# Performance work log

Measured on AMD Instinct MI355X. Metric: run time of the kernel, lower is better.

## Reference

```python
import jax, jax.numpy as jnp
import numpy as np

H, D, E, FOCAL, HID = 8, 32, 16, 4, 256  # heads, att_size, edge types, focal heads, hidden
SCALE = D ** -0.5
B, N = 16, 512


def setup_inputs() -> dict:
    key = jax.random.key(0)
    ks = jax.random.split(key, 16)
    f = lambda i, shape, s=1.0: jax.random.normal(ks[i], shape, jnp.float32) * s
    return {
        "q": f(0, (B, N, HID)),
        "k": f(1, (B, N, HID)),
        "v": f(2, (B, N, HID)),
        "query_edge_emb": f(3, (E, H * D), 0.1),
        "key_edge_emb": f(4, (E, H * D), 0.1),
        "edge_attr": jax.random.randint(ks[5], (B, N, N), 0, E),
        "mask": jax.random.randint(ks[6], (B, N), 0, 2).astype(bool),
        "focal_mask": jax.random.randint(ks[7], (B, N, N), 0, 2).astype(bool),
        "Wq": f(8, (H * D, HID), 0.05), "bq": jnp.zeros((H * D,), jnp.float32),
        "Wk": f(9, (H * D, HID), 0.05), "bk": jnp.zeros((H * D,), jnp.float32),
        "Wv": f(10, (H * D, HID), 0.05), "bv": jnp.zeros((H * D,), jnp.float32),
        "Wo": f(11, (HID, H * D), 0.05), "bo": jnp.zeros((HID,), jnp.float32),
    }


def reference(q, k, v, query_edge_emb, key_edge_emb, edge_attr, mask, focal_mask,
              Wq, bq, Wk, bk, Wv, bv, Wo, bo):
    b, n, _ = q.shape
    # projections -> [B, H, N, D]
    qh = (q @ Wq.T + bq).reshape(b, n, H, D).transpose(0, 2, 1, 3)
    kh = (k @ Wk.T + bk).reshape(b, n, H, D).transpose(0, 2, 1, 3)
    vh = (v @ Wv.T + bv).reshape(b, n, H, D).transpose(0, 2, 1, 3)

    # edge-type embeddings -> [H, E, D]
    qe_emb = query_edge_emb.reshape(E, H, D).transpose(1, 0, 2)
    ke_emb = key_edge_emb.reshape(E, H, D).transpose(1, 0, 2)

    # per-node score against each edge type: [B, H, N, E]
    qe = jnp.einsum('bhnd,hed->bhne', qh, qe_emb)
    ke = jnp.einsum('bhnd,hed->bhne', kh, ke_emb)

    # gather per edge type id: [B, H, N, N]
    idx = jnp.broadcast_to(edge_attr[:, None, :, :], (b, H, n, n))
    edge_bias = jnp.take_along_axis(qe, idx, axis=3) + jnp.take_along_axis(ke, idx, axis=3)

    attn = (jnp.einsum('bhid,bhjd->bhij', qh, kh) + edge_bias) * SCALE

    gh = H - FOCAL
    m_g = jnp.broadcast_to(mask[:, None, None, :], (b, gh, n, n))
    m_f = jnp.broadcast_to(focal_mask[:, None, :, :], (b, FOCAL, n, n))
    m = jnp.concatenate([m_g, m_f], axis=1)
    attn = jnp.where(m, attn, -jnp.inf)
    attn = jax.nn.softmax(attn, axis=3)

    out = jnp.einsum('bhij,bhjd->bhid', attn, vh)
    out = out.transpose(0, 2, 1, 3).reshape(b, n, H * D)
    return out @ Wo.T + bo
```

## Files before the change

kernel.cpp:

```cpp
#include <hip/hip_runtime.h>
#include <math.h>

namespace {

constexpr int B = 16, N = 512, H = 8, D = 32, E = 16, HID = 256;
constexpr float SCALE = 0.17677669529663687f;
constexpr size_t HSZ = (size_t)B * H * N * D;
constexpr size_t WSZ = (size_t)HID * HID;
constexpr int CONV_BLOCKS = 6400;

typedef __attribute__((ext_vector_type(8))) short short8;
typedef __attribute__((ext_vector_type(4))) float float4v;

__device__ inline short f2bf(float x) {
  union { float f; unsigned u; } v; v.f = x;
  unsigned r = v.u + 0x7fffu + ((v.u >> 16) & 1u);
  return (short)(r >> 16);
}

__global__ __launch_bounds__(256) void prep_kernel(
    const float* __restrict__ q, const float* __restrict__ k, const float* __restrict__ v,
    const float* __restrict__ Wq, const float* __restrict__ Wk,
    const float* __restrict__ Wv, const float* __restrict__ Wo,
    unsigned short* __restrict__ qx, unsigned short* __restrict__ kx,
    unsigned short* __restrict__ vx, unsigned short* __restrict__ wq,
    unsigned short* __restrict__ wk, unsigned short* __restrict__ wv,
    unsigned short* __restrict__ wo,
    const int* __restrict__ ea, const void* __restrict__ maskp,
    const void* __restrict__ fmaskp, unsigned char* __restrict__ packed)
{
  __shared__ unsigned char tl[16 * 520];
  __shared__ unsigned sdet[4];
  const int bid = blockIdx.x, t = threadIdx.x;

  if (bid < CONV_BLOCKS) {
    constexpr size_t H4 = HSZ / 4;
    constexpr size_t W4 = WSZ / 4;
    const size_t idx = (size_t)bid * 256 + t;
    const float* src; unsigned short* dst; size_t off;
    if (idx < H4)            { src = q; dst = qx; off = idx; }
    else if (idx < 2 * H4)   { src = k; dst = kx; off = idx - H4; }
    else if (idx < 3 * H4)   { src = v; dst = vx; off = idx - 2 * H4; }
    else {
      const size_t r = idx - 3 * H4;
      const int wsel = (int)(r / W4); off = r % W4;
      src = (wsel == 0) ? Wq : (wsel == 1) ? Wk : (wsel == 2) ? Wv : Wo;
      dst = (wsel == 0) ? wq : (wsel == 1) ? wk : (wsel == 2) ? wv : wo;
    }
    const float4 f = ((const float4*)src)[off];
    ushort4 o;
    o.x = (unsigned short)f2bf(f.x); o.y = (unsigned short)f2bf(f.y);
    o.z = (unsigned short)f2bf(f.z); o.w = (unsigned short)f2bf(f.w);
    ((ushort4*)dst)[off] = o;
    return;
  }

  const int pb = bid - CONV_BLOCKS;
  const int it = pb & 31, b = pb >> 5;
  const int i0 = it * 16;
  const int w = t >> 6, lane = t & 63;
  const unsigned* fm_u = (const unsigned*)fmaskp;
  unsigned o = 0;
#pragma unroll
  for (int i = 0; i < 4; ++i) o |= fm_u[t + i * 256];
  o |= __shfl_xor(o, 1);  o |= __shfl_xor(o, 2);  o |= __shfl_xor(o, 4);
  o |= __shfl_xor(o, 8);  o |= __shfl_xor(o, 16); o |= __shfl_xor(o, 32);
  if (lane == 0) sdet[w] = o;
  __syncthreads();
  const int bf = ((sdet[0] | sdet[1] | sdet[2] | sdet[3]) > 1u) ? 1 : 0;

  const int* fm32 = (const int*)fmaskp;
  const unsigned char* fm8 = (const unsigned char*)fmaskp;
  const int* mk32 = (const int*)maskp;
  const unsigned char* mk8 = (const unsigned char*)maskp;

  for (int idx4 = t; idx4 < 2048; idx4 += 256) {
    const int m = idx4 >> 7, j4 = (idx4 & 127) * 4;
    const size_t rowoff = ((size_t)(b * N) + i0 + m) * N;
    const int4 e4 = *(const int4*)(ea + rowoff + j4);
    int fv0, fv1, fv2, fv3, mv0, mv1, mv2, mv3;
    if (bf) {
      const unsigned fw = *(const unsigned*)(fm8 + rowoff + j4);
      fv0 = fw & 0xff; fv1 = (fw >> 8) & 0xff; fv2 = (fw >> 16) & 0xff; fv3 = fw >> 24;
      const unsigned mw = *(const unsigned*)(mk8 + b * N + j4);
      mv0 = mw & 0xff; mv1 = (mw >> 8) & 0xff; mv2 = (mw >> 16) & 0xff; mv3 = mw >> 24;
    } else {
      const int4 fw = *(const int4*)(fm32 + rowoff + j4);
      fv0 = fw.x; fv1 = fw.y; fv2 = fw.z; fv3 = fw.w;
      const int4 mw = *(const int4*)(mk32 + b * N + j4);
      mv0 = mw.x; mv1 = mw.y; mv2 = mw.z; mv3 = mw.w;
    }
    const unsigned b0 = (e4.x & 15) | (fv0 ? 16u : 0u) | (mv0 ? 32u : 0u);
    const unsigned b1 = (e4.y & 15) | (fv1 ? 16u : 0u) | (mv1 ? 32u : 0u);
    const unsigned b2 = (e4.z & 15) | (fv2 ? 16u : 0u) | (mv2 ? 32u : 0u);
    const unsigned b3 = (e4.w & 15) | (fv3 ? 16u : 0u) | (mv3 ? 32u : 0u);
    *(unsigned*)&tl[m * 520 + j4] = b0 | (b1 << 8) | (b2 << 16) | (b3 << 24);
  }
  __syncthreads();
#pragma unroll
  for (int rep = 0; rep < 2; ++rep) {
    const int j = t * 2 + rep;
    unsigned wd[4];
#pragma unroll
    for (int g = 0; g < 4; ++g) {
      const unsigned c0 = tl[(g * 4 + 0) * 520 + j];
      const unsigned c1 = tl[(g * 4 + 1) * 520 + j];
      const unsigned c2 = tl[(g * 4 + 2) * 520 + j];
      const unsigned c3 = tl[(g * 4 + 3) * 520 + j];
      wd[g] = c0 | (c1 << 8) | (c2 << 16) | (c3 << 24);
    }
    *(uint4*)(packed + ((size_t)(b * 32 + it) * 512 + j) * 16) =
        make_uint4(wd[0], wd[1], wd[2], wd[3]);
  }
}

__global__ __launch_bounds__(256) void gemm_qkv(
    const unsigned short* __restrict__ Xq, const unsigned short* __restrict__ Xk,
    const unsigned short* __restrict__ Xv,
    const unsigned short* __restrict__ Wq, const unsigned short* __restrict__ Wk,
    const unsigned short* __restrict__ Wv,
    const float* __restrict__ bq, const float* __restrict__ bk,
    const float* __restrict__ bv,
    unsigned short* __restrict__ qh, unsigned short* __restrict__ kh,
    unsigned short* __restrict__ vt)
{
  __shared__ __align__(16) unsigned short As[64][72];
  __shared__ __align__(16) unsigned short Bs[64][72];
  const int z = blockIdx.z;
  const unsigned short* X = (z == 0) ? Xq : (z == 1) ? Xk : Xv;
  const unsigned short* W = (z == 0) ? Wq : (z == 1) ? Wk : Wv;
  const float* bias = (z == 0) ? bq : (z == 1) ? bk : bv;

  const int m0 = blockIdx.x * 64, n0 = blockIdx.y * 64;
  const int t = threadIdx.x, lane = t & 63, w = t >> 6;
  const int quad = lane >> 4, col = lane & 15;
  const int wm = (w & 1) * 32, wn = (w >> 1) * 32;
  const int srow = t >> 2, skk = (t & 3) * 16;
  float4v acc[2][2] = {{{0,0,0,0},{0,0,0,0}},{{0,0,0,0},{0,0,0,0}}};

  for (int kit = 0; kit < 4; ++kit) {
    const int k0 = kit * 64;
    {
      const unsigned short* xp = X + (size_t)(m0 + srow) * HID + k0 + skk;
      const unsigned short* wp = W + (size_t)(n0 + srow) * HID + k0 + skk;
      *(short8*)&As[srow][skk] = *(const short8*)xp;
      *(short8*)&As[srow][skk + 8] = *(const short8*)(xp + 8);
      *(short8*)&Bs[srow][skk] = *(const short8*)wp;
      *(short8*)&Bs[srow][skk + 8] = *(const short8*)(wp + 8);
    }
    __syncthreads();
#pragma unroll
    for (int ks = 0; ks < 2; ++ks) {
      const int kk = ks * 32 + quad * 8;
      short8 a0 = *(const short8*)&As[wm + col][kk];
      short8 a1 = *(const short8*)&As[wm + 16 + col][kk];
      short8 b0 = *(const short8*)&Bs[wn + col][kk];
      short8 b1 = *(const short8*)&Bs[wn + 16 + col][kk];
      acc[0][0] = __builtin_amdgcn_mfma_f32_16x16x32_bf16(a0, b0, acc[0][0], 0, 0, 0);
      acc[0][1] = __builtin_amdgcn_mfma_f32_16x16x32_bf16(a0, b1, acc[0][1], 0, 0, 0);
      acc[1][0] = __builtin_amdgcn_mfma_f32_16x16x32_bf16(a1, b0, acc[1][0], 0, 0, 0);
      acc[1][1] = __builtin_amdgcn_mfma_f32_16x16x32_bf16(a1, b1, acc[1][1], 0, 0, 0);
    }
    __syncthreads();
  }
  if (z == 2) {
#pragma unroll
    for (int mt = 0; mt < 2; ++mt)
#pragma unroll
      for (int nt = 0; nt < 2; ++nt)
#pragma unroll
        for (int r = 0; r < 4; ++r) {
          const int m_l = wm + mt * 16 + quad * 4 + r;
          const int n_l = wn + nt * 16 + col;
          As[n_l][m_l] = (unsigned short)f2bf(acc[mt][nt][r] + bias[n0 + n_l]);
        }
    __syncthreads();
#pragma unroll
    for (int rep = 0; rep < 16; ++rep) {
      const int flat = rep * 256 + t;
      const int n_l = flat >> 6, m_l = flat & 63;
      const int n = n0 + n_l, m = m0 + m_l;
      const int b_ = m >> 9, ii = m & 511, h_ = n >> 5, d_ = n & 31;
      vt[((size_t)(b_ * H + h_) * D + d_) * N + ii] = As[n_l][m_l];
    }
    return;
  }
#pragma unroll
  for (int mt = 0; mt < 2; ++mt)
#pragma unroll
    for (int nt = 0; nt < 2; ++nt)
#pragma unroll
      for (int r = 0; r < 4; ++r) {
        const int m = m0 + wm + mt * 16 + quad * 4 + r;
        const int n = n0 + wn + nt * 16 + col;
        const float val = acc[mt][nt][r] + bias[n];
        const int b_ = m >> 9, ii = m & 511, h_ = n >> 5, d_ = n & 31;
        unsigned short* Yh = (z == 0) ? qh : kh;
        Yh[((size_t)(b_ * H + h_) * N + ii) * D + d_] = (unsigned short)f2bf(val);
      }
}

__global__ __launch_bounds__(256) void gemm_out(
    const unsigned short* __restrict__ X, const unsigned short* __restrict__ W,
    const float* __restrict__ bias, float* __restrict__ Yf)
{
  __shared__ __align__(16) unsigned short As[64][72];
  __shared__ __align__(16) unsigned short Bs[64][72];
  const int m0 = blockIdx.x * 64, n0 = blockIdx.y * 64;
  const int t = threadIdx.x, lane = t & 63, w = t >> 6;
  const int quad = lane >> 4, col = lane & 15;
  const int wm = (w & 1) * 32, wn = (w >> 1) * 32;
  const int srow = t >> 2, skk = (t & 3) * 16;
  float4v acc[2][2] = {{{0,0,0,0},{0,0,0,0}},{{0,0,0,0},{0,0,0,0}}};

  for (int kit = 0; kit < 4; ++kit) {
    const int k0 = kit * 64;
    {
      const unsigned short* xp = X + (size_t)(m0 + srow) * HID + k0 + skk;
      const unsigned short* wp = W + (size_t)(n0 + srow) * HID + k0 + skk;
      *(short8*)&As[srow][skk] = *(const short8*)xp;
      *(short8*)&As[srow][skk + 8] = *(const short8*)(xp + 8);
      *(short8*)&Bs[srow][skk] = *(const short8*)wp;
      *(short8*)&Bs[srow][skk + 8] = *(const short8*)(wp + 8);
    }
    __syncthreads();
#pragma unroll
    for (int ks = 0; ks < 2; ++ks) {
      const int kk = ks * 32 + quad * 8;
      short8 a0 = *(const short8*)&As[wm + col][kk];
      short8 a1 = *(const short8*)&As[wm + 16 + col][kk];
      short8 b0 = *(const short8*)&Bs[wn + col][kk];
      short8 b1 = *(const short8*)&Bs[wn + 16 + col][kk];
      acc[0][0] = __builtin_amdgcn_mfma_f32_16x16x32_bf16(a0, b0, acc[0][0], 0, 0, 0);
      acc[0][1] = __builtin_amdgcn_mfma_f32_16x16x32_bf16(a0, b1, acc[0][1], 0, 0, 0);
      acc[1][0] = __builtin_amdgcn_mfma_f32_16x16x32_bf16(a1, b0, acc[1][0], 0, 0, 0);
      acc[1][1] = __builtin_amdgcn_mfma_f32_16x16x32_bf16(a1, b1, acc[1][1], 0, 0, 0);
    }
    __syncthreads();
  }
#pragma unroll
  for (int mt = 0; mt < 2; ++mt)
#pragma unroll
    for (int nt = 0; nt < 2; ++nt)
#pragma unroll
      for (int r = 0; r < 4; ++r) {
        const int m = m0 + wm + mt * 16 + quad * 4 + r;
        const int n = n0 + wn + nt * 16 + col;
        Yf[(size_t)m * HID + n] = acc[mt][nt][r] + bias[n];
      }
}

__global__ __launch_bounds__(256) void attn_mfma(
    const unsigned short* __restrict__ qh, const unsigned short* __restrict__ kh,
    const unsigned short* __restrict__ vt,
    const float* __restrict__ qemb, const float* __restrict__ kemb,
    const unsigned char* __restrict__ packed, unsigned short* __restrict__ ctx)
{
  __shared__ __align__(16) unsigned char SMEM[4][4352];
  __shared__ float qesS[2][16][17];
  __shared__ float2 wlm[4][2][16];
  __shared__ float scl[4][32];
  __shared__ float linv[32];

  const int it = blockIdx.x, p = blockIdx.y, b = blockIdx.z;
  const int i0 = it * 16;
  const int t = threadIdx.x, w = t >> 6, lane = t & 63;
  const int quad = lane >> 4, col = lane & 15;

  unsigned short* Pw = (unsigned short*)&SMEM[w][0];

  unsigned pk[8];
  {
    const unsigned char* pt = packed + ((size_t)(b * 32 + it) * 512) * 16;
#pragma unroll
    for (int c = 0; c < 8; ++c)
      pk[c] = *(const unsigned*)(pt + (size_t)(w * 128 + c * 16 + col) * 16 + quad * 4);
  }

  if (w < 2) {
    const int h2w = w;
    const int hp = p + h2w * 4;
    const int bhw = b * H + hp;
    const short8 qa = *(const short8*)(qh + ((size_t)bhw * N + i0 + col) * D + quad * 8);
    const short8 ka = *(const short8*)(kh + ((size_t)bhw * N + i0 + col) * D + quad * 8);
    const float* eqp = qemb + col * 256 + hp * 32 + quad * 8;
    const float* ekp = kemb + col * 256 + hp * 32 + quad * 8;
    const float4 e1 = *(const float4*)eqp, e2 = *(const float4*)(eqp + 4);
    const float4 k1 = *(const float4*)ekp, k2 = *(const float4*)(ekp + 4);
    short8 eb, kb;
    eb[0]=f2bf(e1.x); eb[1]=f2bf(e1.y); eb[2]=f2bf(e1.z); eb[3]=f2bf(e1.w);
    eb[4]=f2bf(e2.x); eb[5]=f2bf(e2.y); eb[6]=f2bf(e2.z); eb[7]=f2bf(e2.w);
    kb[0]=f2bf(k1.x); kb[1]=f2bf(k1.y); kb[2]=f2bf(k1.z); kb[3]=f2bf(k1.w);
    kb[4]=f2bf(k2.x); kb[5]=f2bf(k2.y); kb[6]=f2bf(k2.z); kb[7]=f2bf(k2.w);
    float4v qe = {0, 0, 0, 0};
    qe = __builtin_amdgcn_mfma_f32_16x16x32_bf16(qa, eb, qe, 0, 0, 0);
    qe = __builtin_amdgcn_mfma_f32_16x16x32_bf16(ka, kb, qe, 0, 0, 0);
#pragma unroll
    for (int r = 0; r < 4; ++r)
      qesS[h2w][quad * 4 + r][col] = qe[r] * SCALE;
  }
  __syncthreads();

  float4v oa[2][2] = {{{0,0,0,0},{0,0,0,0}},{{0,0,0,0},{0,0,0,0}}};
#pragma unroll
  for (int h2 = 0; h2 < 2; ++h2) {
    const int bh = b * H + p + h2 * 4;
    const short8 qf = *(const short8*)(qh + ((size_t)bh * N + i0 + col) * D + quad * 8);

    float s[8][4];
#pragma unroll
    for (int c = 0; c < 8; ++c) {
      const int j0 = w * 128 + c * 16;
      const short8 kf = *(const short8*)(kh + ((size_t)bh * N + j0 + col) * D + quad * 8);
      float4v sc = {0, 0, 0, 0};
      sc = __builtin_amdgcn_mfma_f32_16x16x32_bf16(qf, kf, sc, 0, 0, 0);
#pragma unroll
      for (int r = 0; r < 4; ++r) {
        const int m = quad * 4 + r;
        const unsigned by = pk[c] >> (8 * r);
        const int e = by & 15;
        const int valid = h2 ? (by >> 4) & 1 : (by >> 5) & 1;
        const float sv = fmaf(sc[r], SCALE, qesS[h2][m][e]);
        s[c][r] = valid ? sv : -INFINITY;
      }
    }

    float mW[4];
#pragma unroll
    for (int r = 0; r < 4; ++r) {
      float m2 = s[0][r];
#pragma unroll
      for (int c = 1; c < 8; ++c) m2 = fmaxf(m2, s[c][r]);
      m2 = fmaxf(m2, __shfl_xor(m2, 1));
      m2 = fmaxf(m2, __shfl_xor(m2, 2));
      m2 = fmaxf(m2, __shfl_xor(m2, 4));
      m2 = fmaxf(m2, __shfl_xor(m2, 8));
      mW[r] = fmaxf(m2, -3.0e38f);
    }
#pragma unroll
    for (int r = 0; r < 4; ++r) {
      const int m = quad * 4 + r;
      float sm = 0.f;
#pragma unroll
      for (int c = 0; c < 8; ++c) {
        const float ex = __expf(s[c][r] - mW[r]);
        sm += ex;
        Pw[m * 136 + c * 16 + col] = (unsigned short)f2bf(ex);
      }
      sm += __shfl_xor(sm, 1);
      sm += __shfl_xor(sm, 2);
      sm += __shfl_xor(sm, 4);
      sm += __shfl_xor(sm, 8);
      if (col == 0) wlm[w][h2][m] = make_float2(mW[r], sm);
    }

#pragma unroll
    for (int c2 = 0; c2 < 4; ++c2) {
      const int kl = c2 * 32 + quad * 8;
      const short8 pf = *(const short8*)&Pw[col * 136 + kl];
      const int kg = w * 128 + kl;
      const short8 v0 = *(const short8*)(vt + ((size_t)bh * D + col) * N + kg);
      const short8 v1 = *(const short8*)(vt + ((size_t)bh * D + 16 + col) * N + kg);
      oa[h2][0] = __builtin_amdgcn_mfma_f32_16x16x32_bf16(pf, v0, oa[h2][0], 0, 0, 0);
      oa[h2][1] = __builtin_amdgcn_mfma_f32_16x16x32_bf16(pf, v1, oa[h2][1], 0, 0, 0);
    }
  }
  __syncthreads();

  {
    float* Ow = (float*)&SMEM[w][0];
#pragma unroll
    for (int h2 = 0; h2 < 2; ++h2)
#pragma unroll
      for (int r = 0; r < 4; ++r) {
        const int m = quad * 4 + r;
        Ow[(h2 * 16 + m) * 33 + col] = oa[h2][0][r];
        Ow[(h2 * 16 + m) * 33 + col + 16] = oa[h2][1][r];
      }
  }
  __syncthreads();

  if (t < 128) {
    const int u = t & 3, row = t >> 2, h2 = row >> 4, q = row & 15;
    const float2 s0 = wlm[0][h2][q], s1 = wlm[1][h2][q];
    const float2 s2 = wlm[2][h2][q], s3 = wlm[3][h2][q];
    const float mg = fmaxf(fmaxf(s0.x, s1.x), fmaxf(s2.x, s3.x));
    const float2 sw = (u == 0) ? s0 : (u == 1) ? s1 : (u == 2) ? s2 : s3;
    scl[u][row] = __expf(sw.x - mg);
    if (u == 0) {
      const float ls = s0.y * __expf(s0.x - mg) + s1.y * __expf(s1.x - mg) +
                       s2.y * __expf(s2.x - mg) + s3.y * __expf(s3.x - mg);
      linv[row] = 1.0f / ls;
    }
  }
  __syncthreads();

#pragma unroll
  for (int it2 = 0; it2 < 4; ++it2) {
    const int flat = it2 * 256 + t;
    const int h2 = flat >> 9, rem = flat & 511, q2 = rem >> 5, d = rem & 31;
    const int row = h2 * 16 + q2;
    float val = 0.f;
#pragma unroll
    for (int u = 0; u < 4; ++u)
      val += ((const float*)&SMEM[u][0])[(h2 * 16 + q2) * 33 + d] * scl[u][row];
    ctx[((size_t)(b * N) + i0 + q2) * HID + (p + h2 * 4) * D + d] =
        (unsigned short)f2bf(val * linv[row]);
  }
}

}

extern "C" void kernel_launch(void* const* d_in, const int* in_sizes, int n_in,
                              void* d_out, int out_size, void* d_ws, size_t ws_size,
                              hipStream_t stream)
{
  const float* q    = (const float*)d_in[0];
  const float* k    = (const float*)d_in[1];
  const float* v    = (const float*)d_in[2];
  const float* qemb = (const float*)d_in[3];
  const float* kemb = (const float*)d_in[4];
  const int*   ea   = (const int*)d_in[5];
  const void*  mask = d_in[6];
  const void*  fmask= d_in[7];
  const float* Wq = (const float*)d_in[8];
  const float* bq = (const float*)d_in[9];
  const float* Wk = (const float*)d_in[10];
  const float* bk = (const float*)d_in[11];
  const float* Wv = (const float*)d_in[12];
  const float* bv = (const float*)d_in[13];
  const float* Wo = (const float*)d_in[14];
  const float* bo = (const float*)d_in[15];

  unsigned short* ws16 = (unsigned short*)d_ws;
  unsigned short* qhb = ws16;
  unsigned short* khb = qhb + HSZ;
  unsigned short* vtb = khb + HSZ;
  unsigned short* ctx = vtb + HSZ;
  unsigned char* packed = (unsigned char*)(ctx + (size_t)B * N * HID);
  unsigned short* qxb = (unsigned short*)(packed + (size_t)B * N * N);
  unsigned short* kxb = qxb + HSZ;
  unsigned short* vxb = kxb + HSZ;
  unsigned short* wqb = vxb + HSZ;
  unsigned short* wkb = wqb + WSZ;
  unsigned short* wvb = wkb + WSZ;
  unsigned short* wob = wvb + WSZ;

  prep_kernel<<<CONV_BLOCKS + 512, 256, 0, stream>>>(
      q, k, v, Wq, Wk, Wv, Wo, qxb, kxb, vxb, wqb, wkb, wvb, wob,
      ea, mask, fmask, packed);
  gemm_qkv<<<dim3((B * N) / 64, HID / 64, 3), 256, 0, stream>>>(
      qxb, kxb, vxb, wqb, wkb, wvb, bq, bk, bv, qhb, khb, vtb);
  attn_mfma<<<dim3(N / 16, H / 2, B), 256, 0, stream>>>(qhb, khb, vtb, qemb,
                                                        kemb, packed, ctx);
  gemm_out<<<dim3((B * N) / 64, HID / 64), 256, 0, stream>>>(ctx, wob, bo, (float*)d_out);
}
```

Baseline: 190.5 us.

## Assign one head per attention block and compute edge biases per wave

```diff
diff --git a/kernel.cpp b/kernel.cpp
--- a/kernel.cpp
+++ b/kernel.cpp
@@ -256,18 +256,19 @@
     const float* __restrict__ qemb, const float* __restrict__ kemb,
     const unsigned char* __restrict__ packed, unsigned short* __restrict__ ctx)
 {
-  __shared__ __align__(16) unsigned char SMEM[4][4352];
-  __shared__ float qesS[2][16][17];
-  __shared__ float2 wlm[4][2][16];
-  __shared__ float scl[4][32];
-  __shared__ float linv[32];
-
-  const int it = blockIdx.x, p = blockIdx.y, b = blockIdx.z;
-  const int i0 = it * 16;
+  __shared__ __align__(16) unsigned char SMEM[4][5440];
+  __shared__ float2 wlm[4][16];
+  __shared__ float scl[4][16];
+  __shared__ float linv[16];
+
+  const int it = blockIdx.x, h = blockIdx.y, b = blockIdx.z;
+  const int i0 = it * 16, bh = b * H + h;
   const int t = threadIdx.x, w = t >> 6, lane = t & 63;
   const int quad = lane >> 4, col = lane & 15;
+  const int mbit = (h < 4) ? 5 : 4;
 
   unsigned short* Pw = (unsigned short*)&SMEM[w][0];
+  float* qesW = (float*)&SMEM[w][4352];
 
   unsigned pk[8];
   {
@@ -277,14 +278,12 @@
       pk[c] = *(const unsigned*)(pt + (size_t)(w * 128 + c * 16 + col) * 16 + quad * 4);
   }
 
-  if (w < 2) {
-    const int h2w = w;
-    const int hp = p + h2w * 4;
-    const int bhw = b * H + hp;
-    const short8 qa = *(const short8*)(qh + ((size_t)bhw * N + i0 + col) * D + quad * 8);
-    const short8 ka = *(const short8*)(kh + ((size_t)bhw * N + i0 + col) * D + quad * 8);
-    const float* eqp = qemb + col * 256 + hp * 32 + quad * 8;
-    const float* ekp = kemb + col * 256 + hp * 32 + quad * 8;
+  const short8 qf = *(const short8*)(qh + ((size_t)bh * N + i0 + col) * D + quad * 8);
+
+  {
+    const short8 ka = *(const short8*)(kh + ((size_t)bh * N + i0 + col) * D + quad * 8);
+    const float* eqp = qemb + col * 256 + h * 32 + quad * 8;
+    const float* ekp = kemb + col * 256 + h * 32 + quad * 8;
     const float4 e1 = *(const float4*)eqp, e2 = *(const float4*)(eqp + 4);
     const float4 k1 = *(const float4*)ekp, k2 = *(const float4*)(ekp + 4);
     short8 eb, kb;
@@ -293,119 +292,108 @@
     kb[0]=f2bf(k1.x); kb[1]=f2bf(k1.y); kb[2]=f2bf(k1.z); kb[3]=f2bf(k1.w);
     kb[4]=f2bf(k2.x); kb[5]=f2bf(k2.y); kb[6]=f2bf(k2.z); kb[7]=f2bf(k2.w);
     float4v qe = {0, 0, 0, 0};
-    qe = __builtin_amdgcn_mfma_f32_16x16x32_bf16(qa, eb, qe, 0, 0, 0);
+    qe = __builtin_amdgcn_mfma_f32_16x16x32_bf16(qf, eb, qe, 0, 0, 0);
     qe = __builtin_amdgcn_mfma_f32_16x16x32_bf16(ka, kb, qe, 0, 0, 0);
 #pragma unroll
     for (int r = 0; r < 4; ++r)
-      qesS[h2w][quad * 4 + r][col] = qe[r] * SCALE;
-  }
-  __syncthreads();
-
-  float4v oa[2][2] = {{{0,0,0,0},{0,0,0,0}},{{0,0,0,0},{0,0,0,0}}};
-#pragma unroll
-  for (int h2 = 0; h2 < 2; ++h2) {
-    const int bh = b * H + p + h2 * 4;
-    const short8 qf = *(const short8*)(qh + ((size_t)bh * N + i0 + col) * D + quad * 8);
-
-    float s[8][4];
-#pragma unroll
-    for (int c = 0; c < 8; ++c) {
-      const int j0 = w * 128 + c * 16;
-      const short8 kf = *(const short8*)(kh + ((size_t)bh * N + j0 + col) * D + quad * 8);
-      float4v sc = {0, 0, 0, 0};
-      sc = __builtin_amdgcn_mfma_f32_16x16x32_bf16(qf, kf, sc, 0, 0, 0);
-#pragma unroll
-      for (int r = 0; r < 4; ++r) {
-        const int m = quad * 4 + r;
-        const unsigned by = pk[c] >> (8 * r);
-        const int e = by & 15;
-        const int valid = h2 ? (by >> 4) & 1 : (by >> 5) & 1;
-        const float sv = fmaf(sc[r], SCALE, qesS[h2][m][e]);
-        s[c][r] = valid ? sv : -INFINITY;
-      }
-    }
-
-    float mW[4];
-#pragma unroll
-    for (int r = 0; r < 4; ++r) {
-      float m2 = s[0][r];
-#pragma unroll
-      for (int c = 1; c < 8; ++c) m2 = fmaxf(m2, s[c][r]);
-      m2 = fmaxf(m2, __shfl_xor(m2, 1));
-      m2 = fmaxf(m2, __shfl_xor(m2, 2));
-      m2 = fmaxf(m2, __shfl_xor(m2, 4));
-      m2 = fmaxf(m2, __shfl_xor(m2, 8));
-      mW[r] = fmaxf(m2, -3.0e38f);
-    }
+      qesW[(quad * 4 + r) * 17 + col] = qe[r] * SCALE;
+  }
+
+  float s[8][4];
+#pragma unroll
+  for (int c = 0; c < 8; ++c) {
+    const int j0 = w * 128 + c * 16;
+    const short8 kf = *(const short8*)(kh + ((size_t)bh * N + j0 + col) * D + quad * 8);
+    float4v sc = {0, 0, 0, 0};
+    sc = __builtin_amdgcn_mfma_f32_16x16x32_bf16(qf, kf, sc, 0, 0, 0);
 #pragma unroll
     for (int r = 0; r < 4; ++r) {
       const int m = quad * 4 + r;
-      float sm = 0.f;
-#pragma unroll
-      for (int c = 0; c < 8; ++c) {
-        const float ex = __expf(s[c][r] - mW[r]);
-        sm += ex;
-        Pw[m * 136 + c * 16 + col] = (unsigned short)f2bf(ex);
-      }
-      sm += __shfl_xor(sm, 1);
-      sm += __shfl_xor(sm, 2);
-      sm += __shfl_xor(sm, 4);
-      sm += __shfl_xor(sm, 8);
-      if (col == 0) wlm[w][h2][m] = make_float2(mW[r], sm);
-    }
-
-#pragma unroll
-    for (int c2 = 0; c2 < 4; ++c2) {
-      const int kl = c2 * 32 + quad * 8;
-      const short8 pf = *(const short8*)&Pw[col * 136 + kl];
-      const int kg = w * 128 + kl;
-      const short8 v0 = *(const short8*)(vt + ((size_t)bh * D + col) * N + kg);
-      const short8 v1 = *(const short8*)(vt + ((size_t)bh * D + 16 + col) * N + kg);
-      oa[h2][0] = __builtin_amdgcn_mfma_f32_16x16x32_bf16(pf, v0, oa[h2][0], 0, 0, 0);
-      oa[h2][1] = __builtin_amdgcn_mfma_f32_16x16x32_bf16(pf, v1, oa[h2][1], 0, 0, 0);
-    }
-  }
-  __syncthreads();
+      const unsigned by = pk[c] >> (8 * r);
+      const int e = by & 15;
+      const int valid = (by >> mbit) & 1;
+      const float sv = fmaf(sc[r], SCALE, qesW[m * 17 + e]);
+      s[c][r] = valid ? sv : -INFINITY;
+    }
+  }
+
+  float mW[4];
+#pragma unroll
+  for (int r = 0; r < 4; ++r) {
+    float m2 = s[0][r];
+#pragma unroll
+    for (int c = 1; c < 8; ++c) m2 = fmaxf(m2, s[c][r]);
+    m2 = fmaxf(m2, __shfl_xor(m2, 1));
+    m2 = fmaxf(m2, __shfl_xor(m2, 2));
+    m2 = fmaxf(m2, __shfl_xor(m2, 4));
+    m2 = fmaxf(m2, __shfl_xor(m2, 8));
+    mW[r] = fmaxf(m2, -3.0e38f);
+  }
+#pragma unroll
+  for (int r = 0; r < 4; ++r) {
+    const int m = quad * 4 + r;
+    float sm = 0.f;
+#pragma unroll
+    for (int c = 0; c < 8; ++c) {
+      const float ex = __expf(s[c][r] - mW[r]);
+      sm += ex;
+      Pw[m * 136 + c * 16 + col] = (unsigned short)f2bf(ex);
+    }
+    sm += __shfl_xor(sm, 1);
+    sm += __shfl_xor(sm, 2);
+    sm += __shfl_xor(sm, 4);
+    sm += __shfl_xor(sm, 8);
+    if (col == 0) wlm[w][m] = make_float2(mW[r], sm);
+  }
+
+  float4v o0 = {0, 0, 0, 0}, o1 = {0, 0, 0, 0};
+#pragma unroll
+  for (int c2 = 0; c2 < 4; ++c2) {
+    const int kl = c2 * 32 + quad * 8;
+    const short8 pf = *(const short8*)&Pw[col * 136 + kl];
+    const int kg = w * 128 + kl;
+    const short8 v0 = *(const short8*)(vt + ((size_t)bh * D + col) * N + kg);
+    const short8 v1 = *(const short8*)(vt + ((size_t)bh * D + 16 + col) * N + kg);
+    o0 = __builtin_amdgcn_mfma_f32_16x16x32_bf16(pf, v0, o0, 0, 0, 0);
+    o1 = __builtin_amdgcn_mfma_f32_16x16x32_bf16(pf, v1, o1, 0, 0, 0);
+  }
 
   {
     float* Ow = (float*)&SMEM[w][0];
 #pragma unroll
-    for (int h2 = 0; h2 < 2; ++h2)
-#pragma unroll
-      for (int r = 0; r < 4; ++r) {
-        const int m = quad * 4 + r;
-        Ow[(h2 * 16 + m) * 33 + col] = oa[h2][0][r];
-        Ow[(h2 * 16 + m) * 33 + col + 16] = oa[h2][1][r];
-      }
+    for (int r = 0; r < 4; ++r) {
+      const int m = quad * 4 + r;
+      Ow[m * 33 + col] = o0[r];
+      Ow[m * 33 + col + 16] = o1[r];
+    }
   }
   __syncthreads();
 
-  if (t < 128) {
-    const int u = t & 3, row = t >> 2, h2 = row >> 4, q = row & 15;
-    const float2 s0 = wlm[0][h2][q], s1 = wlm[1][h2][q];
-    const float2 s2 = wlm[2][h2][q], s3 = wlm[3][h2][q];
+  if (t < 64) {
+    const int u = t & 3, q2 = t >> 2;
+    const float2 s0 = wlm[0][q2], s1 = wlm[1][q2];
+    const float2 s2 = wlm[2][q2], s3 = wlm[3][q2];
     const float mg = fmaxf(fmaxf(s0.x, s1.x), fmaxf(s2.x, s3.x));
     const float2 sw = (u == 0) ? s0 : (u == 1) ? s1 : (u == 2) ? s2 : s3;
-    scl[u][row] = __expf(sw.x - mg);
+    scl[u][q2] = __expf(sw.x - mg);
     if (u == 0) {
       const float ls = s0.y * __expf(s0.x - mg) + s1.y * __expf(s1.x - mg) +
                        s2.y * __expf(s2.x - mg) + s3.y * __expf(s3.x - mg);
-      linv[row] = 1.0f / ls;
+      linv[q2] = 1.0f / ls;
     }
   }
   __syncthreads();
 
 #pragma unroll
-  for (int it2 = 0; it2 < 4; ++it2) {
-    const int flat = it2 * 256 + t;
-    const int h2 = flat >> 9, rem = flat & 511, q2 = rem >> 5, d = rem & 31;
-    const int row = h2 * 16 + q2;
+  for (int rep = 0; rep < 2; ++rep) {
+    const int flat = rep * 256 + t;
+    const int q2 = flat >> 5, d = flat & 31;
     float val = 0.f;
 #pragma unroll
     for (int u = 0; u < 4; ++u)
-      val += ((const float*)&SMEM[u][0])[(h2 * 16 + q2) * 33 + d] * scl[u][row];
-    ctx[((size_t)(b * N) + i0 + q2) * HID + (p + h2 * 4) * D + d] =
-        (unsigned short)f2bf(val * linv[row]);
+      val += ((const float*)&SMEM[u][0])[q2 * 33 + d] * scl[u][q2];
+    ctx[((size_t)(b * N) + i0 + q2) * HID + h * D + d] =
+        (unsigned short)f2bf(val * linv[q2]);
   }
 }
 
@@ -451,7 +439,7 @@
       ea, mask, fmask, packed);
   gemm_qkv<<<dim3((B * N) / 64, HID / 64, 3), 256, 0, stream>>>(
       qxb, kxb, vxb, wqb, wkb, wvb, bq, bk, bv, qhb, khb, vtb);
-  attn_mfma<<<dim3(N / 16, H / 2, B), 256, 0, stream>>>(qhb, khb, vtb, qemb,
-                                                        kemb, packed, ctx);
+  attn_mfma<<<dim3(N / 16, H, B), 256, 0, stream>>>(qhb, khb, vtb, qemb,
+                                                    kemb, packed, ctx);
   gemm_out<<<dim3((B * N) / 64, HID / 64), 256, 0, stream>>>(ctx, wob, bo, (float*)d_out);
 }
```

Result: faster. 184.6 us (-3.1%).

## Keep edge-bias table in registers via lane shuffles and swizzle attention grid

Applied to the files above, without the earlier changes.

```diff
diff --git a/kernel.cpp b/kernel.cpp
--- a/kernel.cpp
+++ b/kernel.cpp
@@ -256,18 +256,22 @@
     const float* __restrict__ qemb, const float* __restrict__ kemb,
     const unsigned char* __restrict__ packed, unsigned short* __restrict__ ctx)
 {
-  __shared__ __align__(16) unsigned char SMEM[4][4352];
-  __shared__ float qesS[2][16][17];
+  __shared__ __align__(16) unsigned short P[4][16][136];
   __shared__ float2 wlm[4][2][16];
   __shared__ float scl[4][32];
   __shared__ float linv[32];
 
-  const int it = blockIdx.x, p = blockIdx.y, b = blockIdx.z;
+  const int idx = blockIdx.x;
+  const int g = idx & 7, rr0 = idx >> 3;
+  const int bp = g + 8 * (rr0 >> 5);
+  const int it = rr0 & 31;
+  const int b = bp >> 2, p = bp & 3;
+
   const int i0 = it * 16;
   const int t = threadIdx.x, w = t >> 6, lane = t & 63;
   const int quad = lane >> 4, col = lane & 15;
 
-  unsigned short* Pw = (unsigned short*)&SMEM[w][0];
+  unsigned short* Pw = &P[w][0][0];
 
   unsigned pk[8];
   {
@@ -277,12 +281,15 @@
       pk[c] = *(const unsigned*)(pt + (size_t)(w * 128 + c * 16 + col) * 16 + quad * 4);
   }
 
-  if (w < 2) {
-    const int h2w = w;
-    const int hp = p + h2w * 4;
-    const int bhw = b * H + hp;
-    const short8 qa = *(const short8*)(qh + ((size_t)bhw * N + i0 + col) * D + quad * 8);
-    const short8 ka = *(const short8*)(kh + ((size_t)bhw * N + i0 + col) * D + quad * 8);
+  const short8 qf0 = *(const short8*)(qh + ((size_t)(b * H + p) * N + i0 + col) * D + quad * 8);
+  const short8 qf1 = *(const short8*)(qh + ((size_t)(b * H + p + 4) * N + i0 + col) * D + quad * 8);
+
+  float4v qe[2];
+#pragma unroll
+  for (int h2 = 0; h2 < 2; ++h2) {
+    const int hp = p + h2 * 4;
+    const int bh = b * H + hp;
+    const short8 ka = *(const short8*)(kh + ((size_t)bh * N + i0 + col) * D + quad * 8);
     const float* eqp = qemb + col * 256 + hp * 32 + quad * 8;
     const float* ekp = kemb + col * 256 + hp * 32 + quad * 8;
     const float4 e1 = *(const float4*)eqp, e2 = *(const float4*)(eqp + 4);
@@ -292,20 +299,19 @@
     eb[4]=f2bf(e2.x); eb[5]=f2bf(e2.y); eb[6]=f2bf(e2.z); eb[7]=f2bf(e2.w);
     kb[0]=f2bf(k1.x); kb[1]=f2bf(k1.y); kb[2]=f2bf(k1.z); kb[3]=f2bf(k1.w);
     kb[4]=f2bf(k2.x); kb[5]=f2bf(k2.y); kb[6]=f2bf(k2.z); kb[7]=f2bf(k2.w);
-    float4v qe = {0, 0, 0, 0};
-    qe = __builtin_amdgcn_mfma_f32_16x16x32_bf16(qa, eb, qe, 0, 0, 0);
-    qe = __builtin_amdgcn_mfma_f32_16x16x32_bf16(ka, kb, qe, 0, 0, 0);
-#pragma unroll
-    for (int r = 0; r < 4; ++r)
-      qesS[h2w][quad * 4 + r][col] = qe[r] * SCALE;
-  }
-  __syncthreads();
+    float4v acc = {0, 0, 0, 0};
+    acc = __builtin_amdgcn_mfma_f32_16x16x32_bf16(h2 ? qf1 : qf0, eb, acc, 0, 0, 0);
+    acc = __builtin_amdgcn_mfma_f32_16x16x32_bf16(ka, kb, acc, 0, 0, 0);
+#pragma unroll
+    for (int r = 0; r < 4; ++r) acc[r] *= SCALE;
+    qe[h2] = acc;
+  }
 
   float4v oa[2][2] = {{{0,0,0,0},{0,0,0,0}},{{0,0,0,0},{0,0,0,0}}};
 #pragma unroll
   for (int h2 = 0; h2 < 2; ++h2) {
     const int bh = b * H + p + h2 * 4;
-    const short8 qf = *(const short8*)(qh + ((size_t)bh * N + i0 + col) * D + quad * 8);
+    const short8 qf = h2 ? qf1 : qf0;
 
     float s[8][4];
 #pragma unroll
@@ -316,11 +322,11 @@
       sc = __builtin_amdgcn_mfma_f32_16x16x32_bf16(qf, kf, sc, 0, 0, 0);
 #pragma unroll
       for (int r = 0; r < 4; ++r) {
-        const int m = quad * 4 + r;
         const unsigned by = pk[c] >> (8 * r);
         const int e = by & 15;
         const int valid = h2 ? (by >> 4) & 1 : (by >> 5) & 1;
-        const float sv = fmaf(sc[r], SCALE, qesS[h2][m][e]);
+        const float bias = __shfl(qe[h2][r], (lane & 48) | e);
+        const float sv = fmaf(sc[r], SCALE, bias);
         s[c][r] = valid ? sv : -INFINITY;
       }
     }
@@ -365,10 +371,9 @@
       oa[h2][1] = __builtin_amdgcn_mfma_f32_16x16x32_bf16(pf, v1, oa[h2][1], 0, 0, 0);
     }
   }
-  __syncthreads();
 
   {
-    float* Ow = (float*)&SMEM[w][0];
+    float* Ow = (float*)&P[w][0][0];
 #pragma unroll
     for (int h2 = 0; h2 < 2; ++h2)
 #pragma unroll
@@ -403,7 +408,7 @@
     float val = 0.f;
 #pragma unroll
     for (int u = 0; u < 4; ++u)
-      val += ((const float*)&SMEM[u][0])[(h2 * 16 + q2) * 33 + d] * scl[u][row];
+      val += ((const float*)&P[u][0][0])[(h2 * 16 + q2) * 33 + d] * scl[u][row];
     ctx[((size_t)(b * N) + i0 + q2) * HID + (p + h2 * 4) * D + d] =
         (unsigned short)f2bf(val * linv[row]);
   }
@@ -451,7 +456,6 @@
       ea, mask, fmask, packed);
   gemm_qkv<<<dim3((B * N) / 64, HID / 64, 3), 256, 0, stream>>>(
       qxb, kxb, vxb, wqb, wkb, wvb, bq, bk, bv, qhb, khb, vtb);
-  attn_mfma<<<dim3(N / 16, H / 2, B), 256, 0, stream>>>(qhb, khb, vtb, qemb,
-                                                        kemb, packed, ctx);
+  attn_mfma<<<2048, 256, 0, stream>>>(qhb, khb, vtb, qemb, kemb, packed, ctx);
   gemm_out<<<dim3((B * N) / 64, HID / 64), 256, 0, stream>>>(ctx, wob, bo, (float*)d_out);
 }
```

Result: faster. 186.1 us (-2.3%).
